# Kernel tuning notes

Measured on AMD Instinct MI355X. Metric: run time of the kernel, lower is better.

Reference implementation:

```python
import jax, jax.numpy as jnp
import numpy as np

N_NODES = 512   # hidden_dim in the original code == number of graph nodes
SEQ = 64
DIN = 128
HEADS = 4
DOUT = 128
E = 4096
NEG_SLOPE = 0.2
LN_EPS = 1e-5


def _init(key, shape, fan_in):
    return (jax.random.normal(key, shape, jnp.float32) / np.sqrt(fan_in)).astype(jnp.float32)


def setup_inputs() -> dict:
    key = jax.random.key(0)
    ks = jax.random.split(key, 16)
    x = jax.random.normal(ks[0], (N_NODES, SEQ, DIN), jnp.float32)
    src = jax.random.randint(ks[1], (E,), 0, N_NODES, dtype=jnp.int32)
    # guarantee every node has >=1 incoming edge (DGL requires nonzero in-degree)
    dst = jnp.concatenate([
        jnp.arange(N_NODES, dtype=jnp.int32),
        jax.random.randint(ks[2], (E - N_NODES,), 0, N_NODES, dtype=jnp.int32),
    ])
    return {
        "x": x, "src": src, "dst": dst,
        # GATv2 layer 0: DIN -> DIN, 4 heads (separate fc_src / fc_dst, share_weights=False)
        "W1s": _init(ks[3], (DIN, HEADS * DIN), DIN), "b1s": jnp.zeros((HEADS * DIN,), jnp.float32),
        "W1d": _init(ks[4], (DIN, HEADS * DIN), DIN), "b1d": jnp.zeros((HEADS * DIN,), jnp.float32),
        "attn1": _init(ks[5], (HEADS, DIN), DIN),
        # GATv2 layer 1: DIN*HEADS -> DIN, 1 head
        "W2s": _init(ks[6], (HEADS * DIN, DIN), HEADS * DIN), "b2s": jnp.zeros((DIN,), jnp.float32),
        "W2d": _init(ks[7], (HEADS * DIN, DIN), HEADS * DIN), "b2d": jnp.zeros((DIN,), jnp.float32),
        "attn2": _init(ks[8], (1, DIN), DIN),
        # LayerNorm ln0 + final Linear fc
        "gamma": jnp.ones((DIN,), jnp.float32), "beta": jnp.zeros((DIN,), jnp.float32),
        "Wfc": _init(ks[9], (DIN, DOUT), DIN), "bfc": jnp.zeros((DOUT,), jnp.float32),
    }


def _gatv2(h, src, dst, Ws, bs, Wd, bd, attn, n_nodes, heads, d_out):
    """DGL GATv2Conv: h [N, Din] -> [N, heads, d_out]."""
    fs = (h @ Ws + bs).reshape(-1, heads, d_out)   # [N,H,D]
    fd = (h @ Wd + bd).reshape(-1, heads, d_out)
    e = jax.nn.leaky_relu(fs[src] + fd[dst], NEG_SLOPE)     # [E,H,D]
    logits = jnp.einsum('ehd,hd->eh', e, attn)              # [E,H]
    m = jax.ops.segment_max(logits, dst, num_segments=n_nodes)
    ex = jnp.exp(logits - m[dst])
    den = jax.ops.segment_sum(ex, dst, num_segments=n_nodes)
    alpha = ex / den[dst]                                   # edge softmax per dst node
    return jax.ops.segment_sum(alpha[:, :, None] * fs[src], dst, num_segments=n_nodes)


def reference(x, src, dst, W1s, b1s, W1d, b1d, attn1, W2s, b2s, W2d, b2d, attn2, gamma, beta, Wfc, bfc):
    # preprocess: keep channel 0, log10(rest + 1), NaN -> 0
    xp = jnp.concatenate([x[..., :1], jnp.log10(x[..., 1:] + 1.0)], axis=-1)
    xp = jnp.where(jnp.isnan(xp), 0.0, xp)                  # [N, S, DIN]
    h = jnp.transpose(xp, (1, 0, 2))                        # [S, N, DIN] (seq-batched graph copies)
    g1 = jax.vmap(lambda hh: _gatv2(hh, src, dst, W1s, b1s, W1d, b1d, attn1, N_NODES, HEADS, DIN))(h)
    h2 = g1.reshape(SEQ, N_NODES, HEADS * DIN)              # concat heads
    g2 = jax.vmap(lambda hh: _gatv2(hh, src, dst, W2s, b2s, W2d, b2d, attn2, N_NODES, 1, DIN))(h2)
    g = jnp.transpose(g2[:, :, 0, :], (1, 0, 2))            # [N, S, DIN]
    g = jnp.where(jnp.isnan(g), xp, g)
    out = xp + g                                            # residual; dropout is identity in eval
    mu = jnp.mean(out, axis=-1, keepdims=True)
    var = jnp.mean(jnp.square(out - mu), axis=-1, keepdims=True)
    y = (out - mu) / jnp.sqrt(var + LN_EPS) * gamma + beta  # ln0
    return y @ Wfc + bfc                                    # [N, S, DOUT]
```

## Files before the change

kernel.cpp:

```cpp
#include <hip/hip_runtime.h>
#include <cmath>

#define NN    512
#define SEQL  64
#define DIN   128
#define NH    4
#define NE    4096
#define DOUTN 128
#define LOG2E 1.44269504088896340736f

typedef __attribute__((ext_vector_type(4))) float f32x4;
typedef __attribute__((ext_vector_type(8))) short bf16x8;

__device__ __forceinline__ float lrelu(float v) { return v >= 0.f ? v : 0.2f * v; }

__device__ __forceinline__ unsigned short f2bf(float f) {
    union { float f; unsigned u; } x; x.f = f;
    unsigned r = (x.u + 0x7FFFu + ((x.u >> 16) & 1u)) >> 16;
    return (unsigned short)r;
}
__device__ __forceinline__ float bf2f(unsigned short h) {
    union { unsigned u; float f; } x; x.u = ((unsigned)h) << 16;
    return x.f;
}

__global__ __launch_bounds__(256) void preprocess_k(const float* __restrict__ x,
                                                    float* __restrict__ H,
                                                    unsigned short* __restrict__ Hbf) {
    int tid = blockIdx.x * 256 + threadIdx.x;
    int base = tid * 4;
    int d0 = base & 127;
    int s  = (base >> 7) & 63;
    int n  = base >> 13;
    float4 v = *(const float4*)(x + base);
    if (d0 == 0) {
        v.y = log10f(v.y + 1.f); v.z = log10f(v.z + 1.f); v.w = log10f(v.w + 1.f);
    } else {
        v.x = log10f(v.x + 1.f); v.y = log10f(v.y + 1.f);
        v.z = log10f(v.z + 1.f); v.w = log10f(v.w + 1.f);
    }
    if (v.x != v.x) v.x = 0.f;
    if (v.y != v.y) v.y = 0.f;
    if (v.z != v.z) v.z = 0.f;
    if (v.w != v.w) v.w = 0.f;
    size_t off = ((size_t)s * NN + n) * DIN + d0;
    *(float4*)(H + off) = v;
    ushort4 b; b.x = f2bf(v.x); b.y = f2bf(v.y); b.z = f2bf(v.z); b.w = f2bf(v.w);
    *(ushort4*)(Hbf + off) = b;
}

__global__ __launch_bounds__(256) void castw_k(const float* __restrict__ W1s, const float* __restrict__ W1d,
                                               const float* __restrict__ W2s, const float* __restrict__ W2d,
                                               const float* __restrict__ Wfc,
                                               const float* __restrict__ b1s, const float* __restrict__ b1d,
                                               const float* __restrict__ b2s, const float* __restrict__ b2d,
                                               unsigned short* __restrict__ T1sd, unsigned short* __restrict__ T2sd,
                                               unsigned short* __restrict__ Tfc,
                                               float* __restrict__ bc1, float* __restrict__ bc2) {
    int i = blockIdx.x * 256 + threadIdx.x;
    if (i < 131072) {
        int n = i >> 7, k = i & 127;
        T1sd[i] = f2bf(n < 512 ? W1s[k * 512 + n] : W1d[k * 512 + (n - 512)]);
    } else if (i < 262144) {
        int j = i - 131072; int n = j >> 9, k = j & 511;
        T2sd[j] = f2bf(n < 128 ? W2s[k * 128 + n] : W2d[k * 128 + (n - 128)]);
    } else if (i < 278528) {
        int j = i - 262144; int n = j >> 7, k = j & 127;
        Tfc[j] = f2bf(Wfc[k * 128 + n]);
    } else if (i < 279552) {
        int j = i - 278528;
        bc1[j] = j < 512 ? b1s[j] : b1d[j - 512];
    } else if (i < 279808) {
        int j = i - 279552;
        bc2[j] = j < 128 ? b2s[j] : b2d[j - 128];
    }
}

__global__ void csr_init_k(int* counts, int* fill) {
    int t = threadIdx.x;
    counts[t] = 0; fill[t] = 0;
}
__global__ void csr_hist_k(const int* __restrict__ dst, int* counts) {
    int e = blockIdx.x * 256 + threadIdx.x;
    if (e < NE) atomicAdd(&counts[dst[e]], 1);
}
__global__ void csr_scan_k(const int* __restrict__ counts, int* __restrict__ row_ptr) {
    int l = threadIdx.x;
    int c[8]; int lsum = 0;
#pragma unroll
    for (int j = 0; j < 8; ++j) { c[j] = counts[l * 8 + j]; lsum += c[j]; }
    int pre = lsum;
    for (int o = 1; o < 64; o <<= 1) {
        int v = __shfl_up(pre, o);
        if (l >= o) pre += v;
    }
    int acc = pre - lsum;
#pragma unroll
    for (int j = 0; j < 8; ++j) { row_ptr[l * 8 + j] = acc; acc += c[j]; }
    if (l == 63) row_ptr[512] = acc;
}
__global__ void csr_scatter_k(const int* __restrict__ src, const int* __restrict__ dst,
                              const int* __restrict__ row_ptr, int* fill, int* esrc) {
    int e = blockIdx.x * 256 + threadIdx.x;
    if (e < NE) {
        int dn = dst[e];
        int pos = atomicAdd(&fill[dn], 1);
        esrc[row_ptr[dn] + pos] = src[e];
    }
}

template<int MODE>
__global__ __launch_bounds__(256) void gemm_k(const unsigned short* __restrict__ A,
                                              const unsigned short* __restrict__ BT,
                                              const float* __restrict__ bias,
                                              void* __restrict__ C1v, void* __restrict__ C2v,
                                              int M, int N, int K, int s0, int half) {
    __shared__ unsigned short As[8192];
    __shared__ unsigned short Bs[8192];
    int t = threadIdx.x;
    int w = t >> 6, l = t & 63;
    int wr = w >> 1, wc = w & 1;
    int m0 = blockIdx.y * 128, n0 = blockIdx.x * 128;

    f32x4 acc[4][4];
#pragma unroll
    for (int i = 0; i < 4; ++i)
#pragma unroll
        for (int j = 0; j < 4; ++j) acc[i][j] = (f32x4){0.f, 0.f, 0.f, 0.f};

    for (int k0 = 0; k0 < K; k0 += 64) {
        bf16x8 ra[4], rb[4];
#pragma unroll
        for (int r = 0; r < 4; ++r) {
            int q = t * 16 + r * 4096;
            int row = q >> 7;
            int cole = (q & 127) >> 1;
            ra[r] = *(const bf16x8*)(A  + (size_t)(m0 + row) * K + k0 + cole);
            rb[r] = *(const bf16x8*)(BT + (size_t)(n0 + row) * K + k0 + cole);
        }
        __syncthreads();
#pragma unroll
        for (int r = 0; r < 4; ++r) {
            int q = t * 16 + r * 4096;
            int row = q >> 7;
            int phys = (row << 7) | ((q & 127) ^ ((row & 7) << 4));
            *(bf16x8*)((char*)As + phys) = ra[r];
            *(bf16x8*)((char*)Bs + phys) = rb[r];
        }
        __syncthreads();
#pragma unroll
        for (int ks = 0; ks < 2; ++ks) {
            bf16x8 af[4], bfr[4];
#pragma unroll
            for (int i = 0; i < 4; ++i) {
                int row = wr * 64 + i * 16 + (l & 15);
                int colb = (ks * 64 + ((l >> 4) * 16)) ^ ((row & 7) << 4);
                af[i] = *(const bf16x8*)((const char*)As + (row << 7) + colb);
            }
#pragma unroll
            for (int j = 0; j < 4; ++j) {
                int row = wc * 64 + j * 16 + (l & 15);
                int colb = (ks * 64 + ((l >> 4) * 16)) ^ ((row & 7) << 4);
                bfr[j] = *(const bf16x8*)((const char*)Bs + (row << 7) + colb);
            }
#pragma unroll
            for (int i = 0; i < 4; ++i)
#pragma unroll
                for (int j = 0; j < 4; ++j)
                    acc[i][j] = __builtin_amdgcn_mfma_f32_16x16x32_bf16(af[i], bfr[j], acc[i][j], 0, 0, 0);
        }
    }

    float bl[4];
#pragma unroll
    for (int j = 0; j < 4; ++j) bl[j] = bias[n0 + wc * 64 + j * 16 + (l & 15)];
#pragma unroll
    for (int i = 0; i < 4; ++i) {
#pragma unroll
        for (int j = 0; j < 4; ++j) {
            int n = n0 + wc * 64 + j * 16 + (l & 15);
#pragma unroll
            for (int jj = 0; jj < 4; ++jj) {
                int m = m0 + wr * 64 + i * 16 + (l >> 4) * 4 + jj;
                float v = acc[i][j][jj] + bl[j];
                if (MODE == 1) {
                    int sl = m >> 9, node = m & 511;
                    ((float*)C1v)[((size_t)node * SEQL + (s0 + sl)) * DOUTN + n] = v;
                } else if (MODE == 2) {
                    unsigned short* dp = (unsigned short*)(n < half ? C1v : C2v);
                    int nn = n < half ? n : n - half;
                    dp[(size_t)m * half + nn] = f2bf(v);
                } else {
                    ((unsigned short*)C1v)[(size_t)m * N + n] = f2bf(v);
                }
            }
        }
    }
}

__device__ __forceinline__ void s_swizzle(int bid, int sc, int B, int logB, int& s, int& idx) {
    if ((sc & 7) == 0) {
        int xcd = bid & 7;
        int j = bid >> 3;
        int grp = j >> logB;
        idx = j & (B - 1);
        s = grp * 8 + xcd;
    } else {
        s = bid >> logB;
        idx = bid & (B - 1);
    }
}

__global__ __launch_bounds__(256) void fused_l1_k(const unsigned short* __restrict__ FS,
                                                  const unsigned short* __restrict__ FD,
                                                  const int* __restrict__ row_ptr,
                                                  const int* __restrict__ esrc,
                                                  const float* __restrict__ attn,
                                                  unsigned short* __restrict__ G1,
                                                  int sc) {
    int wv = threadIdx.x >> 6, l = threadIdx.x & 63;
    int s, nb;
    s_swizzle(blockIdx.x, sc, 128, 7, s, nb);
    int n = nb * 4 + wv;
    int e0 = row_ptr[n], e1 = row_ptr[n + 1];
    float at[8], fdv[8];
    bf16x8 fdr = *(const bf16x8*)(FD + ((size_t)s * NN + n) * 512 + l * 8);
#pragma unroll
    for (int k = 0; k < 8; ++k) {
        at[k] = attn[l * 8 + k] * LOG2E;
        fdv[k] = bf2f((unsigned short)fdr[k]);
    }
    const unsigned short* fsbase = FS + (size_t)s * NN * 512 + l * 8;
    float m_run = -INFINITY, den = 0.f;
    float acc[8] = {};

    auto process = [&](bf16x8 raw) {
        float fv[8], part = 0.f;
#pragma unroll
        for (int k = 0; k < 8; ++k) {
            fv[k] = bf2f((unsigned short)raw[k]);
            part += at[k] * lrelu(fv[k] + fdv[k]);
        }
        part += __shfl_xor(part, 1);
        part += __shfl_xor(part, 2);
        part += __shfl_xor(part, 4);
        part += __shfl_xor(part, 8);
        if (part > m_run) {
            float sc_ = exp2f(m_run - part);
            den = den * sc_ + 1.f;
#pragma unroll
            for (int k = 0; k < 8; ++k) acc[k] = acc[k] * sc_ + fv[k];
            m_run = part;
        } else {
            float w = exp2f(part - m_run);
            den += w;
#pragma unroll
            for (int k = 0; k < 8; ++k) acc[k] += w * fv[k];
        }
    };

    for (int j = e0; j < e1; j += 4) {
        int rem = e1 - j;
        bf16x8 r0, r1, r2, r3;
        r0 = *(const bf16x8*)(fsbase + (size_t)esrc[j] * 512);
        if (rem > 1) r1 = *(const bf16x8*)(fsbase + (size_t)esrc[j + 1] * 512);
        if (rem > 2) r2 = *(const bf16x8*)(fsbase + (size_t)esrc[j + 2] * 512);
        if (rem > 3) r3 = *(const bf16x8*)(fsbase + (size_t)esrc[j + 3] * 512);
        process(r0);
        if (rem > 1) process(r1);
        if (rem > 2) process(r2);
        if (rem > 3) process(r3);
    }
    float inv = 1.f / den;
    bf16x8 o8;
#pragma unroll
    for (int k = 0; k < 8; ++k) o8[k] = (short)f2bf(acc[k] * inv);
    *(bf16x8*)(G1 + ((size_t)s * NN + n) * 512 + l * 8) = o8;
}

__global__ __launch_bounds__(256) void fused_l2_k(const unsigned short* __restrict__ FS,
                                                  const unsigned short* __restrict__ FD,
                                                  const int* __restrict__ row_ptr,
                                                  const int* __restrict__ esrc,
                                                  const float* __restrict__ attn,
                                                  const float* __restrict__ H,
                                                  const float* __restrict__ gamma,
                                                  const float* __restrict__ beta,
                                                  unsigned short* __restrict__ Y,
                                                  int s0, int sc) {
    int wv = threadIdx.x >> 6, l = threadIdx.x & 63;
    int s, nb;
    s_swizzle(blockIdx.x, sc, 128, 7, s, nb);
    int n = nb * 4 + wv;
    int e0 = row_ptr[n], e1 = row_ptr[n + 1];
    float a0 = attn[l * 2] * LOG2E, a1 = attn[l * 2 + 1] * LOG2E;
    ushort2 fdr = *(const ushort2*)(FD + ((size_t)s * NN + n) * 128 + l * 2);
    float fd0 = bf2f(fdr.x), fd1 = bf2f(fdr.y);
    const unsigned short* fb = FS + (size_t)s * NN * 128 + l * 2;
    float m_run = -INFINITY, den = 0.f, c0 = 0.f, c1 = 0.f;

    auto process = [&](ushort2 uv) {
        float f0 = bf2f(uv.x), f1 = bf2f(uv.y);
        float part = a0 * lrelu(f0 + fd0) + a1 * lrelu(f1 + fd1);
#pragma unroll
        for (int o = 1; o < 64; o <<= 1) part += __shfl_xor(part, o);
        if (part > m_run) {
            float sc_ = exp2f(m_run - part);
            den = den * sc_ + 1.f;
            c0 = c0 * sc_ + f0;
            c1 = c1 * sc_ + f1;
            m_run = part;
        } else {
            float w = exp2f(part - m_run);
            den += w;
            c0 += w * f0;
            c1 += w * f1;
        }
    };

    for (int j = e0; j < e1; j += 4) {
        int rem = e1 - j;
        ushort2 u0, u1, u2, u3;
        u0 = *(const ushort2*)(fb + (size_t)esrc[j] * 128);
        if (rem > 1) u1 = *(const ushort2*)(fb + (size_t)esrc[j + 1] * 128);
        if (rem > 2) u2 = *(const ushort2*)(fb + (size_t)esrc[j + 2] * 128);
        if (rem > 3) u3 = *(const ushort2*)(fb + (size_t)esrc[j + 3] * 128);
        process(u0);
        if (rem > 1) process(u1);
        if (rem > 2) process(u2);
        if (rem > 3) process(u3);
    }
    float inv = 1.f / den;
    float g0 = c0 * inv, g1 = c1 * inv;
    float2 xp = *(const float2*)(H + ((size_t)(s0 + s) * NN + n) * DIN + l * 2);
    if (g0 != g0) g0 = xp.x;
    if (g1 != g1) g1 = xp.y;
    float o0 = xp.x + g0, o1 = xp.y + g1;
    float ssum = o0 + o1, ssq = o0 * o0 + o1 * o1;
#pragma unroll
    for (int o = 32; o > 0; o >>= 1) { ssum += __shfl_xor(ssum, o); ssq += __shfl_xor(ssq, o); }
    float mu  = ssum * (1.f / 128.f);
    float var = ssq * (1.f / 128.f) - mu * mu;
    float rstd = rsqrtf(var + 1e-5f);
    float y0 = (o0 - mu) * rstd * gamma[l * 2]     + beta[l * 2];
    float y1 = (o1 - mu) * rstd * gamma[l * 2 + 1] + beta[l * 2 + 1];
    ushort2 yo; yo.x = f2bf(y0); yo.y = f2bf(y1);
    *(ushort2*)(Y + ((size_t)s * NN + n) * 128 + l * 2) = yo;
}

extern "C" void kernel_launch(void* const* d_in, const int* in_sizes, int n_in,
                              void* d_out, int out_size, void* d_ws, size_t ws_size,
                              hipStream_t stream) {
    const float* x     = (const float*)d_in[0];
    const int*   src   = (const int*)d_in[1];
    const int*   dst   = (const int*)d_in[2];
    const float* W1s   = (const float*)d_in[3];
    const float* b1s   = (const float*)d_in[4];
    const float* W1d   = (const float*)d_in[5];
    const float* b1d   = (const float*)d_in[6];
    const float* attn1 = (const float*)d_in[7];
    const float* W2s   = (const float*)d_in[8];
    const float* b2s   = (const float*)d_in[9];
    const float* W2d   = (const float*)d_in[10];
    const float* b2d   = (const float*)d_in[11];
    const float* attn2 = (const float*)d_in[12];
    const float* gamma = (const float*)d_in[13];
    const float* beta  = (const float*)d_in[14];
    const float* Wfc   = (const float*)d_in[15];
    const float* bfc   = (const float*)d_in[16];
    float* out = (float*)d_out;

    char* p = (char*)d_ws;
    float*          H    = (float*)p;
    unsigned short* Hbf  = (unsigned short*)(p + 16777216);
    unsigned short* T1sd = (unsigned short*)(p + 25165824);
    unsigned short* T2sd = (unsigned short*)(p + 25427968);
    unsigned short* Tfc  = (unsigned short*)(p + 25690112);
    float*          bc1  = (float*)(p + 25722880);
    float*          bc2  = (float*)(p + 25726976);
    int* counts  = (int*)(p + 25728000);
    int* row_ptr = counts + 512;
    int* fill    = row_ptr + 513;
    int* esrc    = fill + 512;
    const size_t base = 25755648;

    int SC = 1;
    const int cand[7] = {64, 32, 16, 8, 4, 2, 1};
    for (int i = 0; i < 7; ++i)
        if (base + (size_t)cand[i] * 1966080ull <= ws_size) { SC = cand[i]; break; }

    unsigned short* FSb  = (unsigned short*)(p + base);
    unsigned short* FDb  = FSb  + (size_t)SC * 262144;
    unsigned short* G1b  = FDb  + (size_t)SC * 262144;
    unsigned short* FS2b = G1b  + (size_t)SC * 262144;
    unsigned short* FD2b = FS2b + (size_t)SC * 65536;
    unsigned short* Ybf  = FD2b + (size_t)SC * 65536;

    preprocess_k<<<4096, 256, 0, stream>>>(x, H, Hbf);
    castw_k<<<1094, 256, 0, stream>>>(W1s, W1d, W2s, W2d, Wfc, b1s, b1d, b2s, b2d,
                                      T1sd, T2sd, Tfc, bc1, bc2);
    csr_init_k<<<1, 512, 0, stream>>>(counts, fill);
    csr_hist_k<<<NE / 256, 256, 0, stream>>>(dst, counts);
    csr_scan_k<<<1, 64, 0, stream>>>(counts, row_ptr);
    csr_scatter_k<<<NE / 256, 256, 0, stream>>>(src, dst, row_ptr, fill, esrc);

    for (int s0 = 0; s0 < SEQL; s0 += SC) {
        const unsigned short* Hc = Hbf + (size_t)s0 * NN * DIN;
        int M = SC * NN;
        gemm_k<2><<<dim3(8, SC * 4), 256, 0, stream>>>(Hc, T1sd, bc1, FSb, FDb, M, 1024, 128, 0, 512);
        fused_l1_k<<<SC * 128, 256, 0, stream>>>(FSb, FDb, row_ptr, esrc, attn1, G1b, SC);
        gemm_k<2><<<dim3(2, SC * 4), 256, 0, stream>>>(G1b, T2sd, bc2, FS2b, FD2b, M, 256, 512, 0, 128);
        fused_l2_k<<<SC * 128, 256, 0, stream>>>(FS2b, FD2b, row_ptr, esrc, attn2,
                                                 H, gamma, beta, Ybf, s0, SC);
        gemm_k<1><<<dim3(1, SC * 4), 256, 0, stream>>>(Ybf, Tfc, bfc, out, nullptr, M, 128, 128, s0, 0);
    }
}
```

Before: 247.9 us.

## Use direct global-to-LDS loads in GEMM, degree-sort nodes, and make softmax branchless

The GEMM tile loads now use global_load_lds, which writes global memory straight into shared memory with a swizzled chunk index, instead of staging through registers. A new kernel bins nodes by in-degree so each block's waves handle nodes of similar degree, which reduces imbalance between waves in the edge-softmax kernels. The online softmax update in both fused layers becomes branchless, using fmax and two exp2 calls per edge in place of a divergent branch. In exchange the code computes one extra exponential per edge and adds an indirection through the order array, which may hurt locality of the FD and output writes.

```diff
diff --git a/kernel.cpp b/kernel.cpp
--- a/kernel.cpp
+++ b/kernel.cpp
@@ -11,6 +11,10 @@
 
 typedef __attribute__((ext_vector_type(4))) float f32x4;
 typedef __attribute__((ext_vector_type(8))) short bf16x8;
+
+#define GLOAD_LDS16(g, l) __builtin_amdgcn_global_load_lds( \
+    (const __attribute__((address_space(1))) unsigned int*)(g), \
+    (__attribute__((address_space(3))) unsigned int*)(l), 16, 0, 0)
 
 __device__ __forceinline__ float lrelu(float v) { return v >= 0.f ? v : 0.2f * v; }
 
@@ -108,6 +112,30 @@
         esrc[row_ptr[dn] + pos] = src[e];
     }
 }
+__global__ void node_sort_k(const int* __restrict__ row_ptr, int* __restrict__ order) {
+    __shared__ int bins[64];
+    __shared__ int starts[64];
+    int t = threadIdx.x;
+    if (t < 64) bins[t] = 0;
+    __syncthreads();
+    int deg = row_ptr[t + 1] - row_ptr[t];
+    int b = deg < 63 ? deg : 63;
+    atomicAdd(&bins[b], 1);
+    __syncthreads();
+    if (t < 64) {
+        int v = bins[t];
+        int pre = v;
+        for (int o = 1; o < 64; o <<= 1) {
+            int u = __shfl_up(pre, o);
+            if (t >= o) pre += u;
+        }
+        starts[t] = pre - v;
+        bins[t] = 0;
+    }
+    __syncthreads();
+    int pos = atomicAdd(&bins[b], 1);
+    order[starts[b] + pos] = t;
+}
 
 template<int MODE>
 __global__ __launch_bounds__(256) void gemm_k(const unsigned short* __restrict__ A,
@@ -129,23 +157,16 @@
         for (int j = 0; j < 4; ++j) acc[i][j] = (f32x4){0.f, 0.f, 0.f, 0.f};
 
     for (int k0 = 0; k0 < K; k0 += 64) {
-        bf16x8 ra[4], rb[4];
-#pragma unroll
-        for (int r = 0; r < 4; ++r) {
-            int q = t * 16 + r * 4096;
-            int row = q >> 7;
-            int cole = (q & 127) >> 1;
-            ra[r] = *(const bf16x8*)(A  + (size_t)(m0 + row) * K + k0 + cole);
-            rb[r] = *(const bf16x8*)(BT + (size_t)(n0 + row) * K + k0 + cole);
-        }
         __syncthreads();
 #pragma unroll
-        for (int r = 0; r < 4; ++r) {
-            int q = t * 16 + r * 4096;
-            int row = q >> 7;
-            int phys = (row << 7) | ((q & 127) ^ ((row & 7) << 4));
-            *(bf16x8*)((char*)As + phys) = ra[r];
-            *(bf16x8*)((char*)Bs + phys) = rb[r];
+        for (int c = 0; c < 4; ++c) {
+            int rows_base = w * 32 + c * 8;
+            int row = rows_base + (l >> 3);
+            int chunk = (l & 7) ^ (row & 7);
+            const unsigned short* ga = A  + (size_t)(m0 + row) * K + k0 + chunk * 8;
+            const unsigned short* gb = BT + (size_t)(n0 + row) * K + k0 + chunk * 8;
+            GLOAD_LDS16(ga, As + rows_base * 64);
+            GLOAD_LDS16(gb, Bs + rows_base * 64);
         }
         __syncthreads();
 #pragma unroll
@@ -215,13 +236,14 @@
                                                   const unsigned short* __restrict__ FD,
                                                   const int* __restrict__ row_ptr,
                                                   const int* __restrict__ esrc,
+                                                  const int* __restrict__ order,
                                                   const float* __restrict__ attn,
                                                   unsigned short* __restrict__ G1,
                                                   int sc) {
     int wv = threadIdx.x >> 6, l = threadIdx.x & 63;
     int s, nb;
     s_swizzle(blockIdx.x, sc, 128, 7, s, nb);
-    int n = nb * 4 + wv;
+    int n = order[nb * 4 + wv];
     int e0 = row_ptr[n], e1 = row_ptr[n + 1];
     float at[8], fdv[8];
     bf16x8 fdr = *(const bf16x8*)(FD + ((size_t)s * NN + n) * 512 + l * 8);
@@ -245,18 +267,13 @@
         part += __shfl_xor(part, 2);
         part += __shfl_xor(part, 4);
         part += __shfl_xor(part, 8);
-        if (part > m_run) {
-            float sc_ = exp2f(m_run - part);
-            den = den * sc_ + 1.f;
-#pragma unroll
-            for (int k = 0; k < 8; ++k) acc[k] = acc[k] * sc_ + fv[k];
-            m_run = part;
-        } else {
-            float w = exp2f(part - m_run);
-            den += w;
-#pragma unroll
-            for (int k = 0; k < 8; ++k) acc[k] += w * fv[k];
-        }
+        float m_new = fmaxf(m_run, part);
+        float sc_ = exp2f(m_run - m_new);
+        float wgt = exp2f(part - m_new);
+        den = den * sc_ + wgt;
+#pragma unroll
+        for (int k = 0; k < 8; ++k) acc[k] = acc[k] * sc_ + wgt * fv[k];
+        m_run = m_new;
     };
 
     for (int j = e0; j < e1; j += 4) {
@@ -282,6 +299,7 @@
                                                   const unsigned short* __restrict__ FD,
                                                   const int* __restrict__ row_ptr,
                                                   const int* __restrict__ esrc,
+                                                  const int* __restrict__ order,
                                                   const float* __restrict__ attn,
                                                   const float* __restrict__ H,
                                                   const float* __restrict__ gamma,
@@ -291,7 +309,7 @@
     int wv = threadIdx.x >> 6, l = threadIdx.x & 63;
     int s, nb;
     s_swizzle(blockIdx.x, sc, 128, 7, s, nb);
-    int n = nb * 4 + wv;
+    int n = order[nb * 4 + wv];
     int e0 = row_ptr[n], e1 = row_ptr[n + 1];
     float a0 = attn[l * 2] * LOG2E, a1 = attn[l * 2 + 1] * LOG2E;
     ushort2 fdr = *(const ushort2*)(FD + ((size_t)s * NN + n) * 128 + l * 2);
@@ -304,18 +322,13 @@
         float part = a0 * lrelu(f0 + fd0) + a1 * lrelu(f1 + fd1);
 #pragma unroll
         for (int o = 1; o < 64; o <<= 1) part += __shfl_xor(part, o);
-        if (part > m_run) {
-            float sc_ = exp2f(m_run - part);
-            den = den * sc_ + 1.f;
-            c0 = c0 * sc_ + f0;
-            c1 = c1 * sc_ + f1;
-            m_run = part;
-        } else {
-            float w = exp2f(part - m_run);
-            den += w;
-            c0 += w * f0;
-            c1 += w * f1;
-        }
+        float m_new = fmaxf(m_run, part);
+        float sc_ = exp2f(m_run - m_new);
+        float wgt = exp2f(part - m_new);
+        den = den * sc_ + wgt;
+        c0 = c0 * sc_ + wgt * f0;
+        c1 = c1 * sc_ + wgt * f1;
+        m_run = m_new;
     };
 
     for (int j = e0; j < e1; j += 4) {
@@ -382,6 +395,7 @@
     int* row_ptr = counts + 512;
     int* fill    = row_ptr + 513;
     int* esrc    = fill + 512;
+    int* order   = esrc + 4096;
     const size_t base = 25755648;
 
     int SC = 1;
@@ -402,15 +416,16 @@
     csr_init_k<<<1, 512, 0, stream>>>(counts, fill);
     csr_hist_k<<<NE / 256, 256, 0, stream>>>(dst, counts);
     csr_scan_k<<<1, 64, 0, stream>>>(counts, row_ptr);
+    node_sort_k<<<1, 512, 0, stream>>>(row_ptr, order);
     csr_scatter_k<<<NE / 256, 256, 0, stream>>>(src, dst, row_ptr, fill, esrc);
 
     for (int s0 = 0; s0 < SEQL; s0 += SC) {
         const unsigned short* Hc = Hbf + (size_t)s0 * NN * DIN;
         int M = SC * NN;
         gemm_k<2><<<dim3(8, SC * 4), 256, 0, stream>>>(Hc, T1sd, bc1, FSb, FDb, M, 1024, 128, 0, 512);
-        fused_l1_k<<<SC * 128, 256, 0, stream>>>(FSb, FDb, row_ptr, esrc, attn1, G1b, SC);
+        fused_l1_k<<<SC * 128, 256, 0, stream>>>(FSb, FDb, row_ptr, esrc, order, attn1, G1b, SC);
         gemm_k<2><<<dim3(2, SC * 4), 256, 0, stream>>>(G1b, T2sd, bc2, FS2b, FD2b, M, 256, 512, 0, 128);
-        fused_l2_k<<<SC * 128, 256, 0, stream>>>(FS2b, FD2b, row_ptr, esrc, attn2,
+        fused_l2_k<<<SC * 128, 256, 0, stream>>>(FS2b, FD2b, row_ptr, esrc, order, attn2,
                                                  H, gamma, beta, Ybf, s0, SC);
         gemm_k<1><<<dim3(1, SC * 4), 256, 0, stream>>>(Ybf, Tfc, bfc, out, nullptr, M, 128, 128, s0, 0);
     }
```

After: 248.2 us. No clear change (+0.1%).
